# Kernel tuning notes

Measured on AMD Instinct MI355X. Metric: run time of the kernel, lower is better.

The kernel has to match this reference:

```python
import jax, jax.numpy as jnp
import numpy as np


def setup_inputs() -> dict:
    key = jax.random.key(0)
    ks = jax.random.split(key, 7)
    C, IC, H, W, B = 512, 256, 64, 64, 8
    N = H * W
    return {
        "x": jax.random.normal(ks[0], (B, C, H, W), dtype=jnp.float32),
        "w_phi": jax.random.normal(ks[1], (IC, C), dtype=jnp.float32) * 0.02,
        "w_theta": jax.random.normal(ks[2], (IC, C), dtype=jnp.float32) * 0.02,
        "w_g": jax.random.normal(ks[3], (IC, C), dtype=jnp.float32) * 0.02,
        "w_mask": jax.random.normal(ks[4], (C, IC), dtype=jnp.float32) * 0.02,
        "pos_embedding": jax.random.normal(ks[5], (1, N, N), dtype=jnp.float32),
        "pos_embedding_decoder": jax.random.normal(ks[6], (1, IC, H, W), dtype=jnp.float32),
    }


def reference(x, w_phi, w_theta, w_g, w_mask, pos_embedding, pos_embedding_decoder):
    b, c, h, w = x.shape
    n = h * w
    xf = x.reshape(b, c, n)  # [b, c, n]
    # 1x1 convs as channel matmuls
    phi = jnp.einsum('oc,bcn->bon', w_phi, xf)      # [b, ic, n]
    theta = jnp.einsum('oc,bcn->bon', w_theta, xf)  # [b, ic, n]
    g = jnp.einsum('oc,bcn->bon', w_g, xf) + pos_embedding_decoder.reshape(1, -1, n)
    g = jnp.swapaxes(g, 1, 2)  # [b, n, ic]
    # attention logits: theta^T @ phi -> [b, n_theta, n_phi], plus learned pos bias
    attn = jnp.einsum('bci,bcj->bij', theta, phi) + pos_embedding
    # NOTE: original softmax is over dim=1 (the theta/query axis), non-standard
    attn = jax.nn.softmax(attn, axis=1)
    y = jnp.einsum('bij,bjc->bic', attn, g)  # [b, n, ic]
    y = jnp.swapaxes(y, 1, 2).reshape(b, -1, n)  # [b, ic, n]
    mask = jnp.einsum('oc,bcn->bon', w_mask, y).reshape(b, c, h, w)
    return mask + x
```

## Files before the change

### kernel.cpp

```cpp
#include <hip/hip_runtime.h>

typedef short bf8 __attribute__((ext_vector_type(8)));
typedef float f32x4 __attribute__((ext_vector_type(4)));
typedef unsigned short us4 __attribute__((ext_vector_type(4)));
typedef unsigned short us8 __attribute__((ext_vector_type(8)));

#define DEVI __device__ __forceinline__

constexpr int NB = 8, NC = 512, NIC = 256, NS = 4096;

constexpr size_t OFF_XT  = 0;
constexpr size_t OFF_RS  = 0;
constexpr size_t OFF_TP  = 33554432;
constexpr size_t OFF_POS = 67108864;
constexpr size_t OFF_G   = 100663296;
constexpr size_t OFF_G2  = 117440512;
constexpr size_t OFF_Y   = 134217728;
constexpr size_t OFF_WTP = 150994944;
constexpr size_t OFF_WG  = 151519232;
constexpr size_t OFF_WM  = 151781376;
constexpr size_t OFF_SP  = 152043520;

DEVI unsigned short f2bf(float f){
  unsigned u = __float_as_uint(f);
  u += 0x7fffu + ((u >> 16) & 1u);
  return (unsigned short)(u >> 16);
}
DEVI float bf2f(unsigned short b){ return __uint_as_float(((unsigned)b) << 16); }

DEVI void gld16(const void* g, void* l){
  __builtin_amdgcn_global_load_lds((const __attribute__((address_space(1))) unsigned int*)g,
                                   (__attribute__((address_space(3))) unsigned int*)l, 16, 0, 0);
}

DEVI void stageT(unsigned short* dst, const unsigned short* src, int ld, int wid, int lane){
  int rl = lane >> 3;
  int ce = ((lane & 7) << 3) ^ (rl << 3);
#pragma unroll
  for (int it = 0; it < 4; ++it){
    int q = wid + it * 4;
    gld16(src + (size_t)(q * 8 + rl) * ld + ce, dst + q * 512);
  }
}

DEVI void zero44(f32x4 (&a)[4][4]){
  f32x4 z = {0.f, 0.f, 0.f, 0.f};
#pragma unroll
  for (int i = 0; i < 4; ++i)
#pragma unroll
    for (int j = 0; j < 4; ++j) a[i][j] = z;
}

template<int NK64>
DEVI void gemm128v(const unsigned short* Ag, int lda, const unsigned short* Bg, int ldb,
                   unsigned short (&As)[2][8192], unsigned short (&Bs)[2][8192],
                   f32x4 (&acc)[4][4], int wid, int lane)
{
  const int wr = wid >> 1, wc = wid & 1;
  stageT(As[0], Ag, lda, wid, lane);
  stageT(Bs[0], Bg, ldb, wid, lane);
  __syncthreads();
  for (int kt = 0; kt < NK64; ++kt){
    int cur = kt & 1;
    if (kt + 1 < NK64){
      stageT(As[cur ^ 1], Ag + (kt + 1) * 64, lda, wid, lane);
      stageT(Bs[cur ^ 1], Bg + (kt + 1) * 64, ldb, wid, lane);
    }
    bf8 a[2][4], b[2][4];
#pragma unroll
    for (int ks = 0; ks < 2; ++ks){
      int cb = ks * 64 + ((lane >> 4) << 4);
#pragma unroll
      for (int f = 0; f < 4; ++f){
        int rA = wr * 64 + f * 16 + (lane & 15);
        a[ks][f] = *(const bf8*)((char*)As[cur] + rA * 128 + (cb ^ ((rA & 7) << 4)));
        int rB = wc * 64 + f * 16 + (lane & 15);
        b[ks][f] = *(const bf8*)((char*)Bs[cur] + rB * 128 + (cb ^ ((rB & 7) << 4)));
      }
    }
    __builtin_amdgcn_s_setprio(1);
#pragma unroll
    for (int ks = 0; ks < 2; ++ks)
#pragma unroll
      for (int i = 0; i < 4; ++i)
#pragma unroll
        for (int j = 0; j < 4; ++j)
          acc[i][j] = __builtin_amdgcn_mfma_f32_16x16x32_bf16(a[ks][i], b[ks][j], acc[i][j], 0, 0, 0);
    __builtin_amdgcn_s_setprio(0);
    __syncthreads();
  }
}


__global__ void k_prep(const float* wphi, const float* wtheta, const float* wgf, const float* wmf,
                       unsigned short* wtp, unsigned short* wgb, unsigned short* wmb){
  int idx = (blockIdx.x * 256 + threadIdx.x) * 4;
  const float* src; unsigned short* dst;
  if (idx < 131072)      { src = wphi + idx;            dst = wtp + idx; }
  else if (idx < 262144) { src = wtheta + (idx - 131072); dst = wtp + idx; }
  else if (idx < 393216) { src = wgf + (idx - 262144);  dst = wgb + (idx - 262144); }
  else                   { src = wmf + (idx - 393216);  dst = wmb + (idx - 393216); }
  f32x4 v = *(const f32x4*)src;
  us4 o;
#pragma unroll
  for (int r = 0; r < 4; ++r) o[r] = f2bf(v[r]);
  *(us4*)dst = o;
}

__global__ void k_pos(const float* pos, unsigned short* posb){
  size_t base = ((size_t)blockIdx.x * 256 + threadIdx.x) * 8;
  f32x4 v0 = *(const f32x4*)&pos[base];
  f32x4 v1 = *(const f32x4*)&pos[base + 4];
  us8 o;
#pragma unroll
  for (int r = 0; r < 4; ++r){ o[r] = f2bf(v0[r]); o[r + 4] = f2bf(v1[r]); }
  *(us8*)&posb[base] = o;
}

__global__ void k_xt(const float* x, unsigned short* xT){
  int b = blockIdx.z, ct = blockIdx.y, nt = blockIdx.x;
  __shared__ float t[64][65];
  int tid = threadIdx.x;
  int c0 = ct * 64, n0 = nt * 64;
  const float* xp = x + (size_t)b * NC * NS;
#pragma unroll
  for (int it = 0; it < 16; ++it){
    int idx = it * 256 + tid; int r = idx >> 6, cc = idx & 63;
    t[r][cc] = xp[(size_t)(c0 + r) * NS + n0 + cc];
  }
  __syncthreads();
  unsigned short* xo = xT + (size_t)b * NS * NC;
#pragma unroll
  for (int it = 0; it < 16; ++it){
    int idx = it * 256 + tid; int r = idx >> 6, cc = idx & 63;
    xo[(size_t)(n0 + r) * NC + c0 + cc] = f2bf(t[cc][r]);
  }
}


__global__ __launch_bounds__(256, 2) void k_tp(const unsigned short* wtp, const unsigned short* xT,
                                               unsigned short* tp){
  int b = blockIdx.z, ot = blockIdx.y, nt = blockIdx.x;
  int tid = threadIdx.x, wid = tid >> 6, lane = tid & 63, wr = wid >> 1, wc = wid & 1;
  __shared__ unsigned short As[2][8192], Bs[2][8192];
  f32x4 acc[4][4]; zero44(acc);
  gemm128v<8>(wtp + (size_t)(ot * 128) * 512, 512,
              xT + ((size_t)b * NS + nt * 128) * 512, 512, As, Bs, acc, wid, lane);
  unsigned short* out = tp + (size_t)b * NS * 512;
#pragma unroll
  for (int fr = 0; fr < 4; ++fr)
#pragma unroll
    for (int fc = 0; fc < 4; ++fc){
      int o0 = ot * 128 + wr * 64 + fr * 16 + ((lane >> 4) << 2);
      int n  = nt * 128 + wc * 64 + fc * 16 + (lane & 15);
      us4 v;
#pragma unroll
      for (int r = 0; r < 4; ++r) v[r] = f2bf(acc[fr][fc][r]);
      *(us4*)&out[(size_t)n * 512 + o0] = v;
    }
}

__global__ __launch_bounds__(256, 2) void k_g(const unsigned short* xT, const unsigned short* wgb,
                                              const float* pdec, unsigned short* gb){
  int b = blockIdx.z, ot = blockIdx.y, nt = blockIdx.x;
  int tid = threadIdx.x, wid = tid >> 6, lane = tid & 63, wr = wid >> 1, wc = wid & 1;
  __shared__ unsigned short As[2][8192], Bs[2][8192];
  f32x4 acc[4][4]; zero44(acc);
  gemm128v<8>(xT + ((size_t)b * NS + nt * 128) * 512, 512,
              wgb + (size_t)(ot * 128) * 512, 512, As, Bs, acc, wid, lane);
#pragma unroll
  for (int fr = 0; fr < 4; ++fr)
#pragma unroll
    for (int fc = 0; fc < 4; ++fc){
      int n0 = nt * 128 + wr * 64 + fr * 16 + ((lane >> 4) << 2);
      int o  = ot * 128 + wc * 64 + fc * 16 + (lane & 15);
      f32x4 pd = *(const f32x4*)&pdec[(size_t)o * NS + n0];
      us4 v;
#pragma unroll
      for (int r = 0; r < 4; ++r) v[r] = f2bf(acc[fr][fc][r] + pd[r]);
      *(us4*)&gb[((size_t)b * NIC + o) * NS + n0] = v;
    }
}

__global__ __launch_bounds__(256, 2) void k_stats(const unsigned short* tp, const unsigned short* posb,
                                                  float* sp){
  int b = blockIdx.z, ih = blockIdx.y, jt = blockIdx.x;
  int tid = threadIdx.x, wid = tid >> 6, lane = tid & 63, wr = wid >> 1, wc = wid & 1;
  __shared__ unsigned short As[2][8192], Bs[2][8192];
  __shared__ float sred[2][2][64];
  float sacc[4][4];
#pragma unroll
  for (int i = 0; i < 4; ++i)
#pragma unroll
    for (int j = 0; j < 4; ++j) sacc[i][j] = 0.f;
  const unsigned short* tpb = tp + (size_t)b * NS * 512;
  const unsigned short* Ag = tpb + (size_t)(jt * 128) * 512;
  for (int it8 = 0; it8 < 8; ++it8){
    int i0 = (ih * 8 + it8) * 128;
    const unsigned short* Bg = tpb + (size_t)i0 * 512 + 256;
    f32x4 acc[4][4]; zero44(acc);
    gemm128v<4>(Ag, 512, Bg, 512, As, Bs, acc, wid, lane);
#pragma unroll
    for (int fr = 0; fr < 4; ++fr)
#pragma unroll
      for (int fc = 0; fc < 4; ++fc){
        int ig  = i0 + wc * 64 + fc * 16 + (lane & 15);
        int jg0 = jt * 128 + wr * 64 + fr * 16 + ((lane >> 4) << 2);
        us4 pv = *(const us4*)&posb[(size_t)ig * NS + jg0];
#pragma unroll
        for (int r = 0; r < 4; ++r)
          sacc[fr][r] += __expf(acc[fr][fc][r] + bf2f(pv[r]));
      }
  }
#pragma unroll
  for (int m = 1; m <= 8; m <<= 1)
#pragma unroll
    for (int fr = 0; fr < 4; ++fr)
#pragma unroll
      for (int r = 0; r < 4; ++r)
        sacc[fr][r] += __shfl_xor(sacc[fr][r], m, 64);
  if ((lane & 15) == 0){
#pragma unroll
    for (int fr = 0; fr < 4; ++fr)
#pragma unroll
      for (int r = 0; r < 4; ++r)
        sred[wr][wc][fr * 16 + ((lane >> 4) << 2) + r] = sacc[fr][r];
  }
  __syncthreads();
  if (tid < 128){
    int jl = tid;
    sp[((size_t)b * 4 + ih) * NS + jt * 128 + jl] = sred[jl >> 6][0][jl & 63] + sred[jl >> 6][1][jl & 63];
  }
}

__global__ void k_rs(const float* sp, float* rs){
  int idx = blockIdx.x * 256 + threadIdx.x;
  int b = idx >> 12, j = idx & 4095;
  const float* spb = sp + (size_t)b * 4 * NS + j;
  rs[idx] = 1.f / (spb[0] + spb[NS] + spb[2 * NS] + spb[3 * NS]);
}

__global__ void k_sg(const unsigned short* gb, const float* rs, unsigned short* g2){
  size_t base = ((size_t)blockIdx.x * 256 + threadIdx.x) * 8;
  int b = (int)(base / ((size_t)NIC * NS));
  int j0 = (int)(base % NS);
  const float* rsb = rs + (size_t)b * NS + j0;
  f32x4 r0 = *(const f32x4*)&rsb[0];
  f32x4 r1 = *(const f32x4*)&rsb[4];
  us8 gv = *(const us8*)&gb[base];
  us8 o;
#pragma unroll
  for (int r = 0; r < 4; ++r){
    o[r]     = f2bf(bf2f(gv[r])     * r0[r]);
    o[r + 4] = f2bf(bf2f(gv[r + 4]) * r1[r]);
  }
  *(us8*)&g2[base] = o;
}

__global__ __launch_bounds__(256, 2) void k_y(const unsigned short* __restrict__ tp,
                                              const unsigned short* __restrict__ posb,
                                              const unsigned short* __restrict__ g2,
                                              unsigned short* __restrict__ yb){
  int b = blockIdx.y, i0 = blockIdx.x * 64;
  int tid = threadIdx.x, wid = tid >> 6, lane = tid & 63;
  int p = wid >> 1, q = wid & 1;
  __shared__ unsigned short Aph[4][128 * 64];
  __shared__ unsigned short El[64 * 128];
  const unsigned short* tpb = tp + (size_t)b * NS * 512;

  bf8 btr[8][2];
#pragma unroll
  for (int kb = 0; kb < 8; ++kb)
#pragma unroll
    for (int fc = 0; fc < 2; ++fc)
      btr[kb][fc] = *(const bf8*)&tpb[(size_t)(i0 + p * 32 + fc * 16 + (lane & 15)) * 512
                                      + 256 + kb * 32 + (lane >> 4) * 8];

  f32x4 yacc[4][4]; zero44(yacc);
  stageT(Aph[0], tpb, 512, wid, lane);
  stageT(Aph[1], tpb + 64, 512, wid, lane);

  const unsigned short* g2b = g2 + (size_t)b * NIC * NS;

  for (int jt = 0; jt < 32; ++jt){
    int j0 = jt * 128;
    const unsigned short* phiBase = tpb + (size_t)j0 * 512;
    const unsigned short* phiNext = tpb + (size_t)(jt < 31 ? j0 + 128 : j0) * 512;
    us4 pv[4][2];
#pragma unroll
    for (int fr = 0; fr < 4; ++fr){
      int jl = q * 64 + fr * 16 + ((lane >> 4) << 2);
#pragma unroll
      for (int fc = 0; fc < 2; ++fc){
        int il = p * 32 + fc * 16 + (lane & 15);
        pv[fr][fc] = *(const us4*)&posb[(size_t)(i0 + il) * NS + j0 + jl];
      }
    }
    f32x4 lacc[4][2];
    {
      f32x4 z = {0.f, 0.f, 0.f, 0.f};
#pragma unroll
      for (int i = 0; i < 4; ++i)
#pragma unroll
        for (int j = 0; j < 2; ++j) lacc[i][j] = z;
    }
#pragma unroll
    for (int ph = 0; ph < 4; ++ph){
      const unsigned short* ssrc = (ph < 2) ? phiBase + (ph + 2) * 64 : phiNext + (ph - 2) * 64;
      stageT(Aph[(ph + 2) & 3], ssrc, 512, wid, lane);
      asm volatile("s_waitcnt vmcnt(32)" ::: "memory");
      __builtin_amdgcn_s_barrier();
      __builtin_amdgcn_sched_barrier(0);
#pragma unroll
      for (int ks = 0; ks < 2; ++ks){
        bf8 a[4];
#pragma unroll
        for (int fr = 0; fr < 4; ++fr){
          int r = q * 64 + fr * 16 + (lane & 15);
          int cbyte = (ks * 64 + ((lane >> 4) << 4)) ^ ((r & 7) << 4);
          a[fr] = *(const bf8*)((char*)Aph[ph] + r * 128 + cbyte);
        }
        __builtin_amdgcn_s_setprio(1);
#pragma unroll
        for (int fr = 0; fr < 4; ++fr)
#pragma unroll
          for (int fc = 0; fc < 2; ++fc)
            lacc[fr][fc] = __builtin_amdgcn_mfma_f32_16x16x32_bf16(a[fr], btr[ph * 2 + ks][fc],
                                                                   lacc[fr][fc], 0, 0, 0);
        __builtin_amdgcn_s_setprio(0);
      }
    }
#pragma unroll
    for (int fr = 0; fr < 4; ++fr)
#pragma unroll
      for (int fc = 0; fc < 2; ++fc){
        int il = p * 32 + fc * 16 + (lane & 15);
        int jl = q * 64 + fr * 16 + ((lane >> 4) << 2);
        us4 ev;
#pragma unroll
        for (int r = 0; r < 4; ++r)
          ev[r] = f2bf(__expf(lacc[fr][fc][r] + bf2f(pv[fr][fc][r])));
        *(us4*)((char*)El + il * 256 + ((jl * 2) ^ ((il & 7) << 4))) = ev;
      }
    __builtin_amdgcn_sched_barrier(0);
    asm volatile("s_waitcnt lgkmcnt(0)" ::: "memory");
    __builtin_amdgcn_s_barrier();
    __builtin_amdgcn_sched_barrier(0);
#pragma unroll
    for (int jk = 0; jk < 4; ++jk){
      bf8 eb[4];
#pragma unroll
      for (int f = 0; f < 4; ++f){
        int ei = f * 16 + (lane & 15);
        int ebt = jk * 64 + ((lane >> 4) << 4);
        eb[f] = *(const bf8*)((char*)El + ei * 256 + (ebt ^ ((ei & 7) << 4)));
      }
      __builtin_amdgcn_s_setprio(1);
#pragma unroll
      for (int cf = 0; cf < 4; ++cf){
        int c = wid * 64 + cf * 16 + (lane & 15);
        bf8 ga = *(const bf8*)&g2b[(size_t)c * NS + j0 + jk * 32 + (lane >> 4) * 8];
#pragma unroll
        for (int f = 0; f < 4; ++f)
          yacc[cf][f] = __builtin_amdgcn_mfma_f32_16x16x32_bf16(ga, eb[f], yacc[cf][f], 0, 0, 0);
      }
      __builtin_amdgcn_s_setprio(0);
    }
  }
  unsigned short* yo = yb + (size_t)b * NS * NIC;
#pragma unroll
  for (int cf = 0; cf < 4; ++cf)
#pragma unroll
    for (int f = 0; f < 4; ++f){
      int c0 = wid * 64 + cf * 16 + ((lane >> 4) << 2);
      int ig = i0 + f * 16 + (lane & 15);
      us4 v;
#pragma unroll
      for (int r = 0; r < 4; ++r) v[r] = f2bf(yacc[cf][f][r]);
      *(us4*)&yo[(size_t)ig * NIC + c0] = v;
    }
}

__global__ __launch_bounds__(256, 2) void k_out(const unsigned short* yb, const unsigned short* wmb,
                                                const float* xg, float* outg){
  int b = blockIdx.z, cot = blockIdx.y, nt = blockIdx.x;
  int tid = threadIdx.x, wid = tid >> 6, lane = tid & 63, wr = wid >> 1, wc = wid & 1;
  __shared__ unsigned short As[2][8192], Bs[2][8192];
  f32x4 acc[4][4]; zero44(acc);
  gemm128v<4>(yb + ((size_t)b * NS + nt * 128) * 256, 256,
              wmb + (size_t)(cot * 128) * 256, 256, As, Bs, acc, wid, lane);
#pragma unroll
  for (int fr = 0; fr < 4; ++fr)
#pragma unroll
    for (int fc = 0; fc < 4; ++fc){
      int n0 = nt * 128 + wr * 64 + fr * 16 + ((lane >> 4) << 2);
      int co = cot * 128 + wc * 64 + fc * 16 + (lane & 15);
      f32x4 xv = *(const f32x4*)&xg[((size_t)b * NC + co) * NS + n0];
      f32x4 ov = acc[fr][fc] + xv;
      *(f32x4*)&outg[((size_t)b * NC + co) * NS + n0] = ov;
    }
}

extern "C" void kernel_launch(void* const* d_in, const int* in_sizes, int n_in,
                              void* d_out, int out_size, void* d_ws, size_t ws_size,
                              hipStream_t stream){
  const float* x      = (const float*)d_in[0];
  const float* wphi   = (const float*)d_in[1];
  const float* wtheta = (const float*)d_in[2];
  const float* wgf    = (const float*)d_in[3];
  const float* wmf    = (const float*)d_in[4];
  const float* pos    = (const float*)d_in[5];
  const float* pdec   = (const float*)d_in[6];
  float* outg = (float*)d_out;
  char* ws = (char*)d_ws;
  unsigned short* xT   = (unsigned short*)(ws + OFF_XT);
  float*          rsv  = (float*)(ws + OFF_RS);
  unsigned short* tp   = (unsigned short*)(ws + OFF_TP);
  unsigned short* posb = (unsigned short*)(ws + OFF_POS);
  unsigned short* gb   = (unsigned short*)(ws + OFF_G);
  unsigned short* g2   = (unsigned short*)(ws + OFF_G2);
  unsigned short* yb   = (unsigned short*)(ws + OFF_Y);
  unsigned short* wtp  = (unsigned short*)(ws + OFF_WTP);
  unsigned short* wgb  = (unsigned short*)(ws + OFF_WG);
  unsigned short* wmb  = (unsigned short*)(ws + OFF_WM);
  float* sp = (float*)(ws + OFF_SP);

  k_prep<<<512, 256, 0, stream>>>(wphi, wtheta, wgf, wmf, wtp, wgb, wmb);
  k_pos<<<8192, 256, 0, stream>>>(pos, posb);
  k_xt<<<dim3(64, 8, 8), 256, 0, stream>>>(x, xT);
  k_tp<<<dim3(32, 4, 8), 256, 0, stream>>>(wtp, xT, tp);
  k_g<<<dim3(32, 2, 8), 256, 0, stream>>>(xT, wgb, pdec, gb);
  k_stats<<<dim3(32, 4, 8), 256, 0, stream>>>(tp, posb, sp);
  k_rs<<<128, 256, 0, stream>>>(sp, rsv);
  k_sg<<<4096, 256, 0, stream>>>(gb, rsv, g2);
  k_y<<<dim3(64, 8), 256, 0, stream>>>(tp, posb, g2, yb);
  k_out<<<dim3(32, 4, 8), 256, 0, stream>>>(yb, wmb, x, outg);
}
```

Measured before the change: 487.2 us.

## Rewrite softmax stats kernel with register-resident phi and streamed theta

The column-sum kernel is restructured to match k_y. Each block keeps a 64-column phi tile in registers and streams all 4096 theta rows through a 4-stage LDS ring, summing exp over the full axis itself. This removes the partial-sum buffer and the separate reciprocal kernel. Both attention kernels also switch to a flat grid with batch in the low bits of the block index, and use tighter vmcnt waits per phase. The risk is that fewer, longer blocks (512 instead of 1024) may lower occupancy and parallelism.

```diff
diff --git a/kernel.cpp b/kernel.cpp
--- a/kernel.cpp
+++ b/kernel.cpp
@@ -19,7 +19,6 @@
 constexpr size_t OFF_WTP = 150994944;
 constexpr size_t OFF_WG  = 151519232;
 constexpr size_t OFF_WM  = 151781376;
-constexpr size_t OFF_SP  = 152043520;
 
 DEVI unsigned short f2bf(float f){
   unsigned u = __float_as_uint(f);
@@ -182,62 +181,115 @@
     }
 }
 
-__global__ __launch_bounds__(256, 2) void k_stats(const unsigned short* tp, const unsigned short* posb,
-                                                  float* sp){
-  int b = blockIdx.z, ih = blockIdx.y, jt = blockIdx.x;
-  int tid = threadIdx.x, wid = tid >> 6, lane = tid & 63, wr = wid >> 1, wc = wid & 1;
-  __shared__ unsigned short As[2][8192], Bs[2][8192];
-  __shared__ float sred[2][2][64];
-  float sacc[4][4];
-#pragma unroll
-  for (int i = 0; i < 4; ++i)
-#pragma unroll
-    for (int j = 0; j < 4; ++j) sacc[i][j] = 0.f;
+__global__ __launch_bounds__(256, 2) void k_stats(const unsigned short* __restrict__ tp,
+                                                  const unsigned short* __restrict__ posb,
+                                                  float* __restrict__ rs){
+  int bid = blockIdx.x;
+  int b = bid & 7, jb0 = (bid >> 3) * 64;
+  int tid = threadIdx.x, wid = tid >> 6, lane = tid & 63;
+  int p = wid >> 1, q = wid & 1, h = lane >> 4, l15 = lane & 15;
+  __shared__ unsigned short Ath[4][128 * 64];
+  __shared__ float red[64];
   const unsigned short* tpb = tp + (size_t)b * NS * 512;
-  const unsigned short* Ag = tpb + (size_t)(jt * 128) * 512;
-  for (int it8 = 0; it8 < 8; ++it8){
-    int i0 = (ih * 8 + it8) * 128;
-    const unsigned short* Bg = tpb + (size_t)i0 * 512 + 256;
-    f32x4 acc[4][4]; zero44(acc);
-    gemm128v<4>(Ag, 512, Bg, 512, As, Bs, acc, wid, lane);
-#pragma unroll
-    for (int fr = 0; fr < 4; ++fr)
-#pragma unroll
-      for (int fc = 0; fc < 4; ++fc){
-        int ig  = i0 + wc * 64 + fc * 16 + (lane & 15);
-        int jg0 = jt * 128 + wr * 64 + fr * 16 + ((lane >> 4) << 2);
-        us4 pv = *(const us4*)&posb[(size_t)ig * NS + jg0];
+
+  bf8 bphi[8][2];
+#pragma unroll
+  for (int kb = 0; kb < 8; ++kb)
+#pragma unroll
+    for (int frj = 0; frj < 2; ++frj)
+      bphi[kb][frj] = *(const bf8*)&tpb[(size_t)(jb0 + p * 32 + frj * 16 + l15) * 512
+                                        + kb * 32 + h * 8];
+
+  float sacc[2][4];
+#pragma unroll
+  for (int a = 0; a < 2; ++a)
+#pragma unroll
+    for (int r = 0; r < 4; ++r) sacc[a][r] = 0.f;
+
+  stageT(Ath[0], tpb + 256, 512, wid, lane);
+  stageT(Ath[1], tpb + 256 + 64, 512, wid, lane);
+
+  for (int it = 0; it < 32; ++it){
+    int i0t = it * 128;
+    const unsigned short* thBase = tpb + (size_t)i0t * 512 + 256;
+    const unsigned short* thNext = tpb + (size_t)(it < 31 ? i0t + 128 : i0t) * 512 + 256;
+    us4 pv[2][4];
+#pragma unroll
+    for (int frj = 0; frj < 2; ++frj)
+#pragma unroll
+      for (int fci = 0; fci < 4; ++fci){
+        int iG = i0t + q * 64 + fci * 16 + l15;
+        int jG = jb0 + p * 32 + frj * 16 + h * 4;
+        pv[frj][fci] = *(const us4*)&posb[(size_t)iG * NS + jG];
+      }
+    f32x4 lacc[2][4];
+    {
+      f32x4 z = {0.f, 0.f, 0.f, 0.f};
+#pragma unroll
+      for (int a = 0; a < 2; ++a)
+#pragma unroll
+        for (int c = 0; c < 4; ++c) lacc[a][c] = z;
+    }
+#pragma unroll
+    for (int ph = 0; ph < 4; ++ph){
+      const unsigned short* ssrc = (ph < 2) ? thBase + (ph + 2) * 64 : thNext + (ph - 2) * 64;
+      stageT(Ath[(ph + 2) & 3], ssrc, 512, wid, lane);
+      if (ph < 2) asm volatile("s_waitcnt vmcnt(16)" ::: "memory");
+      else        asm volatile("s_waitcnt vmcnt(8)"  ::: "memory");
+      __builtin_amdgcn_s_barrier();
+      __builtin_amdgcn_sched_barrier(0);
+#pragma unroll
+      for (int ks = 0; ks < 2; ++ks){
+        bf8 tfr[4];
+#pragma unroll
+        for (int fci = 0; fci < 4; ++fci){
+          int rI = q * 64 + fci * 16 + l15;
+          int cbyte = (ks * 64 + (h << 4)) ^ ((rI & 7) << 4);
+          tfr[fci] = *(const bf8*)((char*)Ath[ph] + rI * 128 + cbyte);
+        }
+        __builtin_amdgcn_s_setprio(1);
+#pragma unroll
+        for (int frj = 0; frj < 2; ++frj)
+#pragma unroll
+          for (int fci = 0; fci < 4; ++fci)
+            lacc[frj][fci] = __builtin_amdgcn_mfma_f32_16x16x32_bf16(bphi[ph * 2 + ks][frj], tfr[fci],
+                                                                     lacc[frj][fci], 0, 0, 0);
+        __builtin_amdgcn_s_setprio(0);
+      }
+    }
+#pragma unroll
+    for (int frj = 0; frj < 2; ++frj)
+#pragma unroll
+      for (int fci = 0; fci < 4; ++fci)
 #pragma unroll
         for (int r = 0; r < 4; ++r)
-          sacc[fr][r] += __expf(acc[fr][fc][r] + bf2f(pv[r]));
-      }
+          sacc[frj][r] += __expf(lacc[frj][fci][r] + bf2f(pv[frj][fci][r]));
   }
 #pragma unroll
   for (int m = 1; m <= 8; m <<= 1)
 #pragma unroll
-    for (int fr = 0; fr < 4; ++fr)
+    for (int frj = 0; frj < 2; ++frj)
 #pragma unroll
       for (int r = 0; r < 4; ++r)
-        sacc[fr][r] += __shfl_xor(sacc[fr][r], m, 64);
-  if ((lane & 15) == 0){
-#pragma unroll
-    for (int fr = 0; fr < 4; ++fr)
+        sacc[frj][r] += __shfl_xor(sacc[frj][r], m, 64);
+  if (q == 0 && l15 == 0){
+#pragma unroll
+    for (int frj = 0; frj < 2; ++frj)
 #pragma unroll
       for (int r = 0; r < 4; ++r)
-        sred[wr][wc][fr * 16 + ((lane >> 4) << 2) + r] = sacc[fr][r];
+        red[p * 32 + frj * 16 + h * 4 + r] = sacc[frj][r];
   }
   __syncthreads();
-  if (tid < 128){
-    int jl = tid;
-    sp[((size_t)b * 4 + ih) * NS + jt * 128 + jl] = sred[jl >> 6][0][jl & 63] + sred[jl >> 6][1][jl & 63];
-  }
-}
-
-__global__ void k_rs(const float* sp, float* rs){
-  int idx = blockIdx.x * 256 + threadIdx.x;
-  int b = idx >> 12, j = idx & 4095;
-  const float* spb = sp + (size_t)b * 4 * NS + j;
-  rs[idx] = 1.f / (spb[0] + spb[NS] + spb[2 * NS] + spb[3 * NS]);
+  if (q == 1 && l15 == 0){
+#pragma unroll
+    for (int frj = 0; frj < 2; ++frj)
+#pragma unroll
+      for (int r = 0; r < 4; ++r){
+        int jl = p * 32 + frj * 16 + h * 4 + r;
+        float s = sacc[frj][r] + red[jl];
+        rs[(size_t)b * NS + jb0 + jl] = 1.f / s;
+      }
+  }
 }
 
 __global__ void k_sg(const unsigned short* gb, const float* rs, unsigned short* g2){
@@ -261,7 +313,8 @@
                                               const unsigned short* __restrict__ posb,
                                               const unsigned short* __restrict__ g2,
                                               unsigned short* __restrict__ yb){
-  int b = blockIdx.y, i0 = blockIdx.x * 64;
+  int bid = blockIdx.x;
+  int b = bid & 7, i0 = (bid >> 3) * 64;
   int tid = threadIdx.x, wid = tid >> 6, lane = tid & 63;
   int p = wid >> 1, q = wid & 1;
   __shared__ unsigned short Aph[4][128 * 64];
@@ -308,7 +361,8 @@
     for (int ph = 0; ph < 4; ++ph){
       const unsigned short* ssrc = (ph < 2) ? phiBase + (ph + 2) * 64 : phiNext + (ph - 2) * 64;
       stageT(Aph[(ph + 2) & 3], ssrc, 512, wid, lane);
-      asm volatile("s_waitcnt vmcnt(32)" ::: "memory");
+      if (ph < 2) asm volatile("s_waitcnt vmcnt(16)" ::: "memory");
+      else        asm volatile("s_waitcnt vmcnt(8)"  ::: "memory");
       __builtin_amdgcn_s_barrier();
       __builtin_amdgcn_sched_barrier(0);
 #pragma unroll
@@ -423,16 +477,14 @@
   unsigned short* wtp  = (unsigned short*)(ws + OFF_WTP);
   unsigned short* wgb  = (unsigned short*)(ws + OFF_WG);
   unsigned short* wmb  = (unsigned short*)(ws + OFF_WM);
-  float* sp = (float*)(ws + OFF_SP);
 
   k_prep<<<512, 256, 0, stream>>>(wphi, wtheta, wgf, wmf, wtp, wgb, wmb);
   k_pos<<<8192, 256, 0, stream>>>(pos, posb);
   k_xt<<<dim3(64, 8, 8), 256, 0, stream>>>(x, xT);
   k_tp<<<dim3(32, 4, 8), 256, 0, stream>>>(wtp, xT, tp);
   k_g<<<dim3(32, 2, 8), 256, 0, stream>>>(xT, wgb, pdec, gb);
-  k_stats<<<dim3(32, 4, 8), 256, 0, stream>>>(tp, posb, sp);
-  k_rs<<<128, 256, 0, stream>>>(sp, rsv);
+  k_stats<<<512, 256, 0, stream>>>(tp, posb, rsv);
   k_sg<<<4096, 256, 0, stream>>>(gb, rsv, g2);
-  k_y<<<dim3(64, 8), 256, 0, stream>>>(tp, posb, g2, yb);
+  k_y<<<512, 256, 0, stream>>>(tp, posb, g2, yb);
   k_out<<<dim3(32, 4, 8), 256, 0, stream>>>(yb, wmb, x, outg);
 }
```

After: 483.5 us. Within noise of the previous version (-0.8%).
